# Kernel optimization log

Hardware: AMD Instinct MI355X
Metric: run time of the kernel (lower is better)

Reference implementation:

```python
import jax, jax.numpy as jnp
import numpy as np

B, D, S, SEQ_MAX = 8, 256, 1024, 1028  # seq_max = 4*seq_len+4 with seq_len=256
EPS = 1e-5


def setup_inputs() -> dict:
    key = jax.random.key(0)
    k1, k2 = jax.random.split(key, 2)
    x = jax.random.normal(k1, (B, D, S), dtype=jnp.float32)
    weight = jax.random.normal(k2, (D, SEQ_MAX, SEQ_MAX), dtype=jnp.float32)
    gamma = jnp.ones((D,), dtype=jnp.float32)   # LayerNorm weight
    beta = jnp.zeros((D,), dtype=jnp.float32)   # LayerNorm bias
    return {"x": x, "weight": weight, "gamma": gamma, "beta": beta}


def reference(x, weight, gamma, beta):
    s = x.shape[2]
    # strictly-causal per-channel mixing matrix (tril, diagonal=-1)
    w = jnp.tril(weight[:, :s, :s], k=-1)            # [d, s, s]
    # c[b,d,i] = sum_w x[b,d,w] * w[d,i,w]
    c = jax.nn.relu(jnp.einsum('bdw,diw->bdi', x, w))  # [b, d, s]
    # bracket(c, x, 0): elementwise multiplicative gating
    y = x + c * x
    # LayerNorm over the channel (d_model) axis, as in permute->LN->permute
    mu = jnp.mean(y, axis=1, keepdims=True)
    var = jnp.mean((y - mu) ** 2, axis=1, keepdims=True)
    yhat = (y - mu) * jax.lax.rsqrt(var + EPS)
    return yhat * gamma[None, :, None] + beta[None, :, None]
```

## Files before the change

kernel.cpp:

```cpp
#include <hip/hip_runtime.h>

#define SM 1028
#define D_ 256
#define S_ 1024
#define B_ 8

__global__ __launch_bounds__(256, 4)
void lie_mix_kernel(const float* __restrict__ x, const float* __restrict__ weight,
                    float* __restrict__ y) {
  int bid = blockIdx.x;
  int d = bid & 255;
  int bi = 3 - (bid >> 8);
  int i0 = bi << 8;

  __shared__ __align__(16) float xs[B_][1040];

  int t = threadIdx.x;
#pragma unroll
  for (int bb = 0; bb < B_; ++bb) {
    const float4* src = (const float4*)(x + ((size_t)bb * D_ + d) * S_);
    *(float4*)&xs[bb][t << 2] = src[t];
  }
  if (t < 32)
    *(float4*)&xs[t >> 2][1024 + ((t & 3) << 2)] = make_float4(0.f, 0.f, 0.f, 0.f);
  __syncthreads();

  int lane = t & 63;
  int wid = t >> 6;
  int wb = i0 + (wid << 6);
  int g = lane >> 2;
  int j = lane & 3;
  int m = g & 3;
  int q = g >> 2;
  int r0 = wb + m + (q << 4);
  int a = (16 - (m << 2)) & 15;

  const float* wptr = weight + ((size_t)d * SM + r0) * SM + a + (j << 2);

  float acc[4][8];
#pragma unroll
  for (int k = 0; k < 4; ++k)
#pragma unroll
    for (int b = 0; b < 8; ++b) acc[k][b] = 0.f;

  if (a > 0) {
    int e_s = a - 16 + (j << 2);
    if (e_s >= 0) {
      float4 xb[8];
#pragma unroll
      for (int b = 0; b < 8; ++b) xb[b] = *(const float4*)&xs[b][e_s];
#pragma unroll
      for (int k = 0; k < 4; ++k) {
        int rk = r0 + (k << 2);
        float4 v = make_float4(0.f, 0.f, 0.f, 0.f);
        if (e_s < rk) v = *(const float4*)(wptr - 16 + (size_t)(k * 4) * SM);
        if (e_s + 1 >= rk) v.y = 0.f;
        if (e_s + 2 >= rk) v.z = 0.f;
        if (e_s + 3 >= rk) v.w = 0.f;
#pragma unroll
        for (int b = 0; b < 8; ++b)
          acc[k][b] += xb[b].x * v.x + xb[b].y * v.y + xb[b].z * v.z + xb[b].w * v.w;
      }
    }
  }

  int F = (r0 - a) >> 4;
  if (F < 0) F = 0;
  for (int c = 0; c < F; ++c) {
    int e = a + (c << 4) + (j << 2);
    float4 wc[4];
#pragma unroll
    for (int k = 0; k < 4; ++k)
      wc[k] = *(const float4*)(wptr + (size_t)(k * 4) * SM + (c << 4));
#pragma unroll
    for (int b = 0; b < 8; ++b) {
      float4 xb = *(const float4*)&xs[b][e];
#pragma unroll
      for (int k = 0; k < 4; ++k) {
        acc[k][b] += xb.x * wc[k].x + xb.y * wc[k].y + xb.z * wc[k].z + xb.w * wc[k].w;
      }
    }
  }

#pragma unroll
  for (int ec = 0; ec < 2; ++ec) {
    int c = F + ec;
    int e_s = a + (c << 4) + (j << 2);
    float4 wm[4];
#pragma unroll
    for (int k = 0; k < 4; ++k) {
      int rk = r0 + (k << 2);
      float4 v = make_float4(0.f, 0.f, 0.f, 0.f);
      if (e_s < rk) v = *(const float4*)(wptr + (size_t)(k * 4) * SM + (c << 4));
      if (e_s + 1 >= rk) v.y = 0.f;
      if (e_s + 2 >= rk) v.z = 0.f;
      if (e_s + 3 >= rk) v.w = 0.f;
      wm[k] = v;
    }
#pragma unroll
    for (int b = 0; b < 8; ++b) {
      float4 xb = *(const float4*)&xs[b][e_s];
#pragma unroll
      for (int k = 0; k < 4; ++k) {
        acc[k][b] += xb.x * wm[k].x + xb.y * wm[k].y + xb.z * wm[k].z + xb.w * wm[k].w;
      }
    }
  }

#pragma unroll
  for (int s = 1; s < 4; s <<= 1)
#pragma unroll
    for (int k = 0; k < 4; ++k)
#pragma unroll
      for (int b = 0; b < 8; ++b)
        acc[k][b] += __shfl_xor(acc[k][b], s, 64);

  {
    int b0 = j, b1 = j + 4;
#pragma unroll
    for (int k = 0; k < 4; ++k) {
      int r = r0 + (k << 2);
      float x0 = xs[b0][r], x1 = xs[b1][r];
      y[((size_t)b0 * D_ + d) * S_ + r] = x0 * (1.f + fmaxf(acc[k][b0], 0.f));
      y[((size_t)b1 * D_ + d) * S_ + r] = x1 * (1.f + fmaxf(acc[k][b1], 0.f));
    }
  }
}

__global__ __launch_bounds__(256)
void ln_kernel(const float* __restrict__ y, const float* __restrict__ gamma,
               const float* __restrict__ beta, float* __restrict__ out) {
  __shared__ float tile[D_][33];
  __shared__ float ps[8][32];
  __shared__ float pq[8][32];
  __shared__ float mu[32];
  __shared__ float rs[32];
  int b = blockIdx.x >> 5;
  int s0 = (blockIdx.x & 31) << 5;
  int t = threadIdx.x;
  int sj = t & 31, dq = t >> 5;
  for (int dd = dq; dd < D_; dd += 8)
    tile[dd][sj] = y[((size_t)b * D_ + dd) * S_ + s0 + sj];
  __syncthreads();
  float sm = 0.f, sq = 0.f;
#pragma unroll 8
  for (int r = 0; r < 32; ++r) {
    float v = tile[dq * 32 + r][sj];
    sm += v;
    sq += v * v;
  }
  ps[dq][sj] = sm;
  pq[dq][sj] = sq;
  __syncthreads();
  if (t < 32) {
    float S = 0.f, Q = 0.f;
#pragma unroll
    for (int qq = 0; qq < 8; ++qq) { S += ps[qq][t]; Q += pq[qq][t]; }
    float mm = S * (1.f / 256.f);
    float var = Q * (1.f / 256.f) - mm * mm;
    mu[t] = mm;
    rs[t] = rsqrtf(var + 1e-5f);
  }
  __syncthreads();
  for (int dd = dq; dd < D_; dd += 8) {
    float v = tile[dd][sj];
    out[((size_t)b * D_ + dd) * S_ + s0 + sj] =
        (v - mu[sj]) * rs[sj] * gamma[dd] + beta[dd];
  }
}

extern "C" void kernel_launch(void* const* d_in, const int* in_sizes, int n_in,
                              void* d_out, int out_size, void* d_ws, size_t ws_size,
                              hipStream_t stream) {
  const float* x = (const float*)d_in[0];
  const float* weight = (const float*)d_in[1];
  const float* gamma = (const float*)d_in[2];
  const float* beta = (const float*)d_in[3];
  float* out = (float*)d_out;
  float* y = (float*)d_ws;

  lie_mix_kernel<<<1024, 256, 0, stream>>>(x, weight, y);
  ln_kernel<<<256, 256, 0, stream>>>(y, gamma, beta, out);
}
```

Measured before the change: 151.3 us.

## Remap lanes so each row group spans 64 contiguous weight columns

Each wavefront now has 16 lanes sharing a row group, and they read 16 consecutive float4s (256 bytes) of a weight row per step, where before 4 lanes read 64 bytes. The four row-quads a lane handled are now processed in a sequential loop, each with its own reduction and store. The intent is more coalesced, wider weight reads from global memory. In exchange each row group needs a 16-lane shuffle reduction, a select tree to pick the output, and ragged tail work at 64-column granularity, which wastes some lanes.

```diff
diff --git a/kernel.cpp b/kernel.cpp
--- a/kernel.cpp
+++ b/kernel.cpp
@@ -28,101 +28,110 @@
   int lane = t & 63;
   int wid = t >> 6;
   int wb = i0 + (wid << 6);
-  int g = lane >> 2;
-  int j = lane & 3;
-  int m = g & 3;
-  int q = g >> 2;
-  int r0 = wb + m + (q << 4);
+  int m = lane >> 4;
+  int j = lane & 15;
   int a = (16 - (m << 2)) & 15;
+  int j4 = j << 2;
 
-  const float* wptr = weight + ((size_t)d * SM + r0) * SM + a + (j << 2);
+  for (int qq = 0; qq < 4; ++qq) {
+    int r0 = wb + m + (qq << 4);
+    const float* wptr = weight + ((size_t)d * SM + r0) * SM + a + j4;
 
-  float acc[4][8];
+    float acc[4][8];
 #pragma unroll
-  for (int k = 0; k < 4; ++k)
+    for (int k = 0; k < 4; ++k)
 #pragma unroll
-    for (int b = 0; b < 8; ++b) acc[k][b] = 0.f;
+      for (int b = 0; b < 8; ++b) acc[k][b] = 0.f;
 
-  if (a > 0) {
-    int e_s = a - 16 + (j << 2);
-    if (e_s >= 0) {
-      float4 xb[8];
+    if (a > 0) {
+      int e_s = a - 64 + j4;
+      if (e_s >= 0) {
+        float4 xb[8];
 #pragma unroll
-      for (int b = 0; b < 8; ++b) xb[b] = *(const float4*)&xs[b][e_s];
+        for (int b = 0; b < 8; ++b) xb[b] = *(const float4*)&xs[b][e_s];
+#pragma unroll
+        for (int k = 0; k < 4; ++k) {
+          int rk = r0 + (k << 2);
+          float4 v = make_float4(0.f, 0.f, 0.f, 0.f);
+          if (e_s < rk) v = *(const float4*)(wptr - 64 + (size_t)(k * 4) * SM);
+          if (e_s + 1 >= rk) v.y = 0.f;
+          if (e_s + 2 >= rk) v.z = 0.f;
+          if (e_s + 3 >= rk) v.w = 0.f;
+#pragma unroll
+          for (int b = 0; b < 8; ++b)
+            acc[k][b] += xb[b].x * v.x + xb[b].y * v.y + xb[b].z * v.z + xb[b].w * v.w;
+        }
+      }
+    }
+
+    int F = (r0 - a) >> 6;
+    if (F < 0) F = 0;
+    for (int c = 0; c < F; ++c) {
+      int w0 = c << 6;
+      float4 wc[4];
+#pragma unroll
+      for (int k = 0; k < 4; ++k)
+        wc[k] = *(const float4*)(wptr + (size_t)(k * 4) * SM + w0);
+      int e = a + w0 + j4;
+#pragma unroll
+      for (int b = 0; b < 8; ++b) {
+        float4 xb = *(const float4*)&xs[b][e];
+#pragma unroll
+        for (int k = 0; k < 4; ++k) {
+          acc[k][b] += xb.x * wc[k].x + xb.y * wc[k].y + xb.z * wc[k].z + xb.w * wc[k].w;
+        }
+      }
+    }
+
+#pragma unroll
+    for (int ec = 0; ec < 2; ++ec) {
+      int w0 = (F + ec) << 6;
+      int e_s = a + w0 + j4;
+      int e_x = e_s > 1024 ? 1024 : e_s;
+      float4 wm[4];
 #pragma unroll
       for (int k = 0; k < 4; ++k) {
         int rk = r0 + (k << 2);
         float4 v = make_float4(0.f, 0.f, 0.f, 0.f);
-        if (e_s < rk) v = *(const float4*)(wptr - 16 + (size_t)(k * 4) * SM);
+        if (e_s < rk) v = *(const float4*)(wptr + (size_t)(k * 4) * SM + w0);
         if (e_s + 1 >= rk) v.y = 0.f;
         if (e_s + 2 >= rk) v.z = 0.f;
         if (e_s + 3 >= rk) v.w = 0.f;
+        wm[k] = v;
+      }
+#pragma unroll
+      for (int b = 0; b < 8; ++b) {
+        float4 xb = *(const float4*)&xs[b][e_x];
+#pragma unroll
+        for (int k = 0; k < 4; ++k) {
+          acc[k][b] += xb.x * wm[k].x + xb.y * wm[k].y + xb.z * wm[k].z + xb.w * wm[k].w;
+        }
+      }
+    }
+
+#pragma unroll
+    for (int s = 1; s < 16; s <<= 1)
+#pragma unroll
+      for (int k = 0; k < 4; ++k)
 #pragma unroll
         for (int b = 0; b < 8; ++b)
-          acc[k][b] += xb[b].x * v.x + xb[b].y * v.y + xb[b].z * v.z + xb[b].w * v.w;
-      }
-    }
-  }
+          acc[k][b] += __shfl_xor(acc[k][b], s, 64);
 
-  int F = (r0 - a) >> 4;
-  if (F < 0) F = 0;
-  for (int c = 0; c < F; ++c) {
-    int e = a + (c << 4) + (j << 2);
-    float4 wc[4];
+    {
+      int kk = j & 3, bb = j >> 2;
+      float v0 = 0.f, v1 = 0.f;
 #pragma unroll
-    for (int k = 0; k < 4; ++k)
-      wc[k] = *(const float4*)(wptr + (size_t)(k * 4) * SM + (c << 4));
+      for (int k = 0; k < 4; ++k)
 #pragma unroll
-    for (int b = 0; b < 8; ++b) {
-      float4 xb = *(const float4*)&xs[b][e];
-#pragma unroll
-      for (int k = 0; k < 4; ++k) {
-        acc[k][b] += xb.x * wc[k].x + xb.y * wc[k].y + xb.z * wc[k].z + xb.w * wc[k].w;
-      }
-    }
-  }
-
-#pragma unroll
-  for (int ec = 0; ec < 2; ++ec) {
-    int c = F + ec;
-    int e_s = a + (c << 4) + (j << 2);
-    float4 wm[4];
-#pragma unroll
-    for (int k = 0; k < 4; ++k) {
-      int rk = r0 + (k << 2);
-      float4 v = make_float4(0.f, 0.f, 0.f, 0.f);
-      if (e_s < rk) v = *(const float4*)(wptr + (size_t)(k * 4) * SM + (c << 4));
-      if (e_s + 1 >= rk) v.y = 0.f;
-      if (e_s + 2 >= rk) v.z = 0.f;
-      if (e_s + 3 >= rk) v.w = 0.f;
-      wm[k] = v;
-    }
-#pragma unroll
-    for (int b = 0; b < 8; ++b) {
-      float4 xb = *(const float4*)&xs[b][e_s];
-#pragma unroll
-      for (int k = 0; k < 4; ++k) {
-        acc[k][b] += xb.x * wm[k].x + xb.y * wm[k].y + xb.z * wm[k].z + xb.w * wm[k].w;
-      }
-    }
-  }
-
-#pragma unroll
-  for (int s = 1; s < 4; s <<= 1)
-#pragma unroll
-    for (int k = 0; k < 4; ++k)
-#pragma unroll
-      for (int b = 0; b < 8; ++b)
-        acc[k][b] += __shfl_xor(acc[k][b], s, 64);
-
-  {
-    int b0 = j, b1 = j + 4;
-#pragma unroll
-    for (int k = 0; k < 4; ++k) {
-      int r = r0 + (k << 2);
-      float x0 = xs[b0][r], x1 = xs[b1][r];
-      y[((size_t)b0 * D_ + d) * S_ + r] = x0 * (1.f + fmaxf(acc[k][b0], 0.f));
-      y[((size_t)b1 * D_ + d) * S_ + r] = x1 * (1.f + fmaxf(acc[k][b1], 0.f));
+        for (int b = 0; b < 4; ++b) {
+          bool sel = (kk == k) && (bb == b);
+          v0 = sel ? acc[k][b] : v0;
+          v1 = sel ? acc[k][b + 4] : v1;
+        }
+      int r = r0 + (kk << 2);
+      float xv0 = xs[bb][r], xv1 = xs[bb + 4][r];
+      y[((size_t)bb * D_ + d) * S_ + r] = xv0 * (1.f + fmaxf(v0, 0.f));
+      y[((size_t)(bb + 4) * D_ + d) * S_ + r] = xv1 * (1.f + fmaxf(v1, 0.f));
     }
   }
 }
```

Measured after the change: 158.6 us. 1.05x slower.
